# Kernel tuning notes

Hardware: AMD Instinct MI355X
Metric: run time of the kernel (lower is better)

Reference implementation:

```python
import jax, jax.numpy as jnp
import numpy as np

N_NODES = 100000
N_EDGES = 3200000
D_IN = 128
D_OUT = 128


def setup_inputs() -> dict:
    key = jax.random.key(0)
    k1, k2, k3, k4 = jax.random.split(key, 4)
    features = jax.random.normal(k1, (N_NODES, D_IN), dtype=jnp.float32)
    src = jax.random.randint(k2, (N_EDGES,), 0, N_NODES, dtype=jnp.int32)
    dst = jax.random.randint(k3, (N_EDGES,), 0, N_NODES, dtype=jnp.int32)
    # nn.Linear params (Kaiming-uniform-ish init scale)
    bound = 1.0 / np.sqrt(D_IN)
    W = jax.random.uniform(k4, (D_IN, D_OUT), dtype=jnp.float32, minval=-bound, maxval=bound)
    b = jnp.zeros((D_OUT,), dtype=jnp.float32)
    return {"features": features, "W": W, "b": b, "src": src, "dst": dst}


def reference(features, W, b, src, dst):
    # message: gather source node features per edge  [E, D_IN]
    msg = features[src]
    # mean_reduce: segment mean over in-edges per destination node
    summed = jax.ops.segment_sum(msg, dst, num_segments=N_NODES)
    deg = jax.ops.segment_sum(jnp.ones((msg.shape[0],), dtype=features.dtype), dst, num_segments=N_NODES)
    deg = deg[:, None]
    # DGL semantics: nodes with no incoming messages keep their original 'h'
    h = jnp.where(deg > 0, summed / jnp.maximum(deg, 1.0), features)
    # node_update: linear + activation applied to all nodes
    return jax.nn.relu(h @ W + b)
```

## Files before the change

### kernel.cpp

```cpp
#include <hip/hip_runtime.h>

#define N_NODES 100000
#define N_EDGES 3200000
#define D 128

#define BSHIFT 8
#define BSIZE  256
#define NBUCK  391
#define CAP    9216
#define PART_TILE 4096
#define NB_PART ((N_EDGES + PART_TILE - 1) / PART_TILE)
#define CPL 7
#define NSTRIPS (N_NODES / 16)
#define FUSE_GRID 2084

#define OFF_GCUR  0
#define OFF_DBASE 512
#define OFF_OFFS  1024
#define OFF_DEG   101024
#define OFF_CSR   201024
#define FEATB_OFF 13604096ULL
#define WPK_OFF   39204096ULL

typedef __attribute__((ext_vector_type(8))) short short8_t;
typedef __attribute__((ext_vector_type(4))) float f32x4;

__device__ __forceinline__ ushort f2bf(float x) {
    unsigned u = __float_as_uint(x);
    unsigned r = u + 0x7FFFu + ((u >> 16) & 1u);
    return (ushort)(r >> 16);
}
__device__ __forceinline__ float blo(unsigned v) { return __uint_as_float(v << 16); }
__device__ __forceinline__ float bhi(unsigned v) { return __uint_as_float(v & 0xFFFF0000u); }

__global__ __launch_bounds__(256) void gcn_cvt_kernel(
    const float* __restrict__ in, ushort* __restrict__ out, int n8)
{
    int i = blockIdx.x * 256 + threadIdx.x;
    if (i >= n8) return;
    const float4* p = (const float4*)in + (size_t)i * 2;
    float4 a = p[0], b = p[1];
    ushort4 r0 = make_ushort4(f2bf(a.x), f2bf(a.y), f2bf(a.z), f2bf(a.w));
    ushort4 r1 = make_ushort4(f2bf(b.x), f2bf(b.y), f2bf(b.z), f2bf(b.w));
    ushort4* q = (ushort4*)out + (size_t)i * 2;
    q[0] = r0;
    q[1] = r1;
}

__global__ __launch_bounds__(256) void gcn_wpack_kernel(
    const float* __restrict__ W, ushort* __restrict__ wpk)
{
    int tid = blockIdx.x * 256 + threadIdx.x;
    if (tid >= 32 * 64) return;
    int f = tid >> 6, l = tid & 63;
    int n4 = f >> 2, k4 = f & 3;
    int col = n4 * 16 + (l & 15);
    int kb  = k4 * 32 + ((l >> 4) << 3);
    ushort* q = wpk + (size_t)tid * 8;
    #pragma unroll
    for (int t = 0; t < 8; ++t) q[t] = f2bf(W[(kb + t) * D + col]);
}

__global__ void gcn_init_kernel(int* __restrict__ gcur)
{
    int t = blockIdx.x * 256 + threadIdx.x;
    if (t < NBUCK) gcur[t] = t * CAP;
}

__global__ __launch_bounds__(256) void gcn_part_kernel(
    const int* __restrict__ src, const int* __restrict__ dst,
    int* __restrict__ gcur, int* __restrict__ part)
{
    __shared__ int cnt[NBUCK];
    __shared__ int lbase[NBUCK + 1];
    __shared__ int gbase[NBUCK];
    __shared__ int stage[PART_TILE];
    __shared__ ushort sbuck[PART_TILE];

    int t = threadIdx.x;
    int eb = blockIdx.x * PART_TILE;
    int nT = N_EDGES - eb; if (nT > PART_TILE) nT = PART_TILE;

    for (int i = t; i < NBUCK; i += 256) cnt[i] = 0;
    __syncthreads();

    #pragma unroll
    for (int it = 0; it < PART_TILE / 256; ++it) {
        int e = it * 256 + t;
        if (e < nT) atomicAdd(&cnt[dst[eb + e] >> BSHIFT], 1);
    }
    __syncthreads();

    if (t < 64) {
        int v[CPL];
        int s = 0;
        #pragma unroll
        for (int j = 0; j < CPL; ++j) {
            int i = t * CPL + j;
            v[j] = (i < NBUCK) ? cnt[i] : 0;
            s += v[j];
        }
        int inc = s;
        #pragma unroll
        for (int d = 1; d < 64; d <<= 1) {
            int up = __shfl_up(inc, d, 64);
            if (t >= d) inc += up;
        }
        int run = inc - s;
        #pragma unroll
        for (int j = 0; j < CPL; ++j) {
            int i = t * CPL + j;
            if (i < NBUCK) lbase[i] = run;
            run += v[j];
        }
        if (t == 63) lbase[NBUCK] = run;
    }
    __syncthreads();

    for (int i = t; i < NBUCK; i += 256) {
        int c = lbase[i + 1] - lbase[i];
        gbase[i] = c ? atomicAdd(&gcur[i], c) : 0;
        cnt[i] = 0;
    }
    __syncthreads();

    #pragma unroll
    for (int it = 0; it < PART_TILE / 256; ++it) {
        int e = it * 256 + t;
        if (e < nT) {
            int dvv = dst[eb + e];
            int svv = src[eb + e];
            int b  = dvv >> BSHIFT;
            int dl = dvv & (BSIZE - 1);
            int pos = lbase[b] + atomicAdd(&cnt[b], 1);
            stage[pos] = (dl << 17) | svv;
            sbuck[pos] = (ushort)b;
        }
    }
    __syncthreads();

    for (int i = t; i < nT; i += 256) {
        int b = sbuck[i];
        part[gbase[b] + (i - lbase[b])] = stage[i];
    }
}

__global__ __launch_bounds__(64) void gcn_bscan_kernel(
    const int* __restrict__ gcur, int* __restrict__ dbase)
{
    int l = threadIdx.x;
    int v[CPL];
    int s = 0;
    #pragma unroll
    for (int j = 0; j < CPL; ++j) {
        int i = CPL * l + j;
        v[j] = (i < NBUCK) ? (gcur[i] - i * CAP) : 0;
        s += v[j];
    }
    int inc = s;
    #pragma unroll
    for (int d = 1; d < 64; d <<= 1) {
        int up = __shfl_up(inc, d, 64);
        if (l >= d) inc += up;
    }
    int run = inc - s;
    #pragma unroll
    for (int j = 0; j < CPL; ++j) {
        int i = CPL * l + j;
        if (i < NBUCK) dbase[i] = run;
        run += v[j];
    }
}

__global__ __launch_bounds__(256) void gcn_bfill_kernel(
    const int* __restrict__ gcur, const int* __restrict__ dbase,
    const int* __restrict__ part, int* __restrict__ csr,
    int* __restrict__ offs, int* __restrict__ deg)
{
    __shared__ int stage[CAP];
    __shared__ int stage2[CAP];
    __shared__ int ldeg[BSIZE];
    __shared__ int lcur[BSIZE];
    __shared__ int wsum[4];
    int k = blockIdx.x, t = threadIdx.x;
    int pb = k * CAP;
    int nE = gcur[k] - pb;
    if (nE > CAP) nE = CAP;
    int db = dbase[k];

    ldeg[t] = 0;
    __syncthreads();
    for (int i = t; i < nE; i += 256) {
        int pk = part[pb + i];
        stage[i] = pk;
        atomicAdd(&ldeg[pk >> 17], 1);
    }
    __syncthreads();

    int lane = t & 63, wid = t >> 6;
    int v = ldeg[t];
    int inc = v;
    #pragma unroll
    for (int d = 1; d < 64; d <<= 1) {
        int up = __shfl_up(inc, d, 64);
        if (lane >= d) inc += up;
    }
    if (lane == 63) wsum[wid] = inc;
    __syncthreads();
    if (t == 0) {
        int c = 0;
        #pragma unroll
        for (int w = 0; w < 4; ++w) { int x = wsum[w]; wsum[w] = c; c += x; }
    }
    __syncthreads();
    int excl = (inc - v) + wsum[wid];
    lcur[t] = excl;
    int node = (k << BSHIFT) + t;
    if (node < N_NODES) { offs[node] = db + excl; deg[node] = v; }
    __syncthreads();

    for (int i = t; i < nE; i += 256) {
        int pk = stage[i];
        int p = atomicAdd(&lcur[pk >> 17], 1);
        stage2[p] = pk & 0x1FFFF;
    }
    __syncthreads();

    for (int i = t; i < nE; i += 256) csr[db + i] = stage2[i];
}

__global__ __launch_bounds__(256) void gcn_fused_kernel(
    const float* __restrict__ feat,
    const ushort* __restrict__ featb,
    const ushort* __restrict__ wpk,
    const float* __restrict__ bias,
    const int* __restrict__ offs,
    const int* __restrict__ deg,
    const int* __restrict__ csr,
    float* __restrict__ out)
{
    int t = threadIdx.x, lane = t & 63, w = t >> 6;

    short8_t wb[8];
    #pragma unroll
    for (int j = 0; j < 8; ++j)
        wb[j] = *(const short8_t*)(wpk + ((size_t)(w * 8 + j) * 64 + lane) * 8);
    float bj[2];
    bj[0] = bias[(2 * w) * 16 + (lane & 15)];
    bj[1] = bias[(2 * w + 1) * 16 + (lane & 15)];

    __shared__ ushort hlds[16 * 136];

    for (int s = blockIdx.x; s < NSTRIPS; s += FUSE_GRID) {
        int m0 = s * 16;
        __syncthreads();

        #pragma unroll
        for (int i = 0; i < 4; ++i) {
            int r = m0 + w * 4 + i;
            int beg = offs[r], dg = deg[r];
            float s0 = 0.0f, s1 = 0.0f;
            if (dg == 0) {
                float2 f2 = *(const float2*)(feat + (size_t)r * D + lane * 2);
                s0 = f2.x; s1 = f2.y;
            } else {
                int p = beg, e = beg + dg;
                for (; p + 8 <= e; p += 8) {
                    int i0 = csr[p],     i1 = csr[p + 1], i2 = csr[p + 2], i3 = csr[p + 3];
                    int i4 = csr[p + 4], i5 = csr[p + 5], i6 = csr[p + 6], i7 = csr[p + 7];
                    unsigned v0 = *(const unsigned*)(featb + ((size_t)i0 << 7) + lane * 2);
                    unsigned v1 = *(const unsigned*)(featb + ((size_t)i1 << 7) + lane * 2);
                    unsigned v2 = *(const unsigned*)(featb + ((size_t)i2 << 7) + lane * 2);
                    unsigned v3 = *(const unsigned*)(featb + ((size_t)i3 << 7) + lane * 2);
                    unsigned v4 = *(const unsigned*)(featb + ((size_t)i4 << 7) + lane * 2);
                    unsigned v5 = *(const unsigned*)(featb + ((size_t)i5 << 7) + lane * 2);
                    unsigned v6 = *(const unsigned*)(featb + ((size_t)i6 << 7) + lane * 2);
                    unsigned v7 = *(const unsigned*)(featb + ((size_t)i7 << 7) + lane * 2);
                    s0 += blo(v0) + blo(v1) + blo(v2) + blo(v3);
                    s1 += bhi(v0) + bhi(v1) + bhi(v2) + bhi(v3);
                    s0 += blo(v4) + blo(v5) + blo(v6) + blo(v7);
                    s1 += bhi(v4) + bhi(v5) + bhi(v6) + bhi(v7);
                }
                for (; p + 4 <= e; p += 4) {
                    int i0 = csr[p], i1 = csr[p + 1], i2 = csr[p + 2], i3 = csr[p + 3];
                    unsigned v0 = *(const unsigned*)(featb + ((size_t)i0 << 7) + lane * 2);
                    unsigned v1 = *(const unsigned*)(featb + ((size_t)i1 << 7) + lane * 2);
                    unsigned v2 = *(const unsigned*)(featb + ((size_t)i2 << 7) + lane * 2);
                    unsigned v3 = *(const unsigned*)(featb + ((size_t)i3 << 7) + lane * 2);
                    s0 += blo(v0) + blo(v1) + blo(v2) + blo(v3);
                    s1 += bhi(v0) + bhi(v1) + bhi(v2) + bhi(v3);
                }
                for (; p < e; ++p) {
                    unsigned v = *(const unsigned*)(featb + ((size_t)csr[p] << 7) + lane * 2);
                    s0 += blo(v); s1 += bhi(v);
                }
                float inv = 1.0f / (float)dg;
                s0 *= inv; s1 *= inv;
            }
            unsigned pk = ((unsigned)f2bf(s1) << 16) | (unsigned)f2bf(s0);
            *(unsigned*)(&hlds[(w * 4 + i) * 136 + lane * 2]) = pk;
        }
        __syncthreads();

        short8_t a[4];
        #pragma unroll
        for (int k4 = 0; k4 < 4; ++k4)
            a[k4] = *(const short8_t*)(&hlds[(lane & 15) * 136 + k4 * 32 + ((lane >> 4) << 3)]);

        #pragma unroll
        for (int nt = 0; nt < 2; ++nt) {
            f32x4 acc = { bj[nt], bj[nt], bj[nt], bj[nt] };
            #pragma unroll
            for (int k4 = 0; k4 < 4; ++k4)
                acc = __builtin_amdgcn_mfma_f32_16x16x32_bf16(a[k4], wb[nt * 4 + k4], acc, 0, 0, 0);
            int col  = (2 * w + nt) * 16 + (lane & 15);
            int rowb = m0 + ((lane >> 4) << 2);
            #pragma unroll
            for (int rr = 0; rr < 4; ++rr)
                out[(size_t)(rowb + rr) * D + col] = fmaxf(acc[rr], 0.0f);
        }
    }
}

extern "C" void kernel_launch(void* const* d_in, const int* in_sizes, int n_in,
                              void* d_out, int out_size, void* d_ws, size_t ws_size,
                              hipStream_t stream) {
    const float* feat = (const float*)d_in[0];
    const float* W    = (const float*)d_in[1];
    const float* bias = (const float*)d_in[2];
    const int*   src  = (const int*)d_in[3];
    const int*   dst  = (const int*)d_in[4];
    float* out = (float*)d_out;

    int* ib     = (int*)d_ws;
    int* gcur   = ib + OFF_GCUR;
    int* dbase  = ib + OFF_DBASE;
    int* offs   = ib + OFF_OFFS;
    int* deg    = ib + OFF_DEG;
    int* csr    = ib + OFF_CSR;
    ushort* featb = (ushort*)((char*)d_ws + FEATB_OFF);
    ushort* wpk   = (ushort*)((char*)d_ws + WPK_OFF);
    int* part = (int*)d_out;

    {
        int n8 = N_NODES * D / 8;
        gcn_cvt_kernel<<<(n8 + 255) / 256, 256, 0, stream>>>(feat, featb, n8);
    }
    gcn_wpack_kernel<<<8, 256, 0, stream>>>(W, wpk);
    gcn_init_kernel<<<2, 256, 0, stream>>>(gcur);
    gcn_part_kernel<<<NB_PART, 256, 0, stream>>>(src, dst, gcur, part);
    gcn_bscan_kernel<<<1, 64, 0, stream>>>(gcur, dbase);
    gcn_bfill_kernel<<<NBUCK, 256, 0, stream>>>(gcur, dbase, part, csr, offs, deg);
    gcn_fused_kernel<<<FUSE_GRID, 256, 0, stream>>>(feat, featb, wpk, bias, offs, deg, csr, out);
}
```

Measured before the change: 319.8 us.

## Fuse per-bucket CSR build into aggregation kernel using smaller 64-node buckets

Removes the separate bucket-scan and bucket-fill kernels. The fused aggregation kernel now takes one 64-node bucket per block, counting-sorts that bucket's edges in LDS and reads neighbour indices from shared memory instead of a global CSR array. This avoids writing and re-reading the CSR, offsets and degree arrays, and saves two launches. In exchange the partition kernel spreads each tile over 1563 buckets instead of 391, so its global scatter is more fragmented; its tile and thread counts are raised to compensate.

```diff
diff --git a/kernel.cpp b/kernel.cpp
--- a/kernel.cpp
+++ b/kernel.cpp
@@ -4,23 +4,19 @@
 #define N_EDGES 3200000
 #define D 128
 
-#define BSHIFT 8
-#define BSIZE  256
-#define NBUCK  391
-#define CAP    9216
-#define PART_TILE 4096
+#define BSHIFT 6
+#define BNODES 64
+#define NBUCK  1563
+#define CAP    2432
+#define PART_TILE 8192
+#define PART_THREADS 512
 #define NB_PART ((N_EDGES + PART_TILE - 1) / PART_TILE)
-#define CPL 7
-#define NSTRIPS (N_NODES / 16)
-#define FUSE_GRID 2084
+#define CPL 25
 
 #define OFF_GCUR  0
-#define OFF_DBASE 512
-#define OFF_OFFS  1024
-#define OFF_DEG   101024
-#define OFF_CSR   201024
-#define FEATB_OFF 13604096ULL
-#define WPK_OFF   39204096ULL
+#define OFF_PART  2048
+#define FEATB_OFF 15213056ULL
+#define WPK_OFF   40813056ULL
 
 typedef __attribute__((ext_vector_type(8))) short short8_t;
 typedef __attribute__((ext_vector_type(4))) float f32x4;
@@ -67,7 +63,7 @@
     if (t < NBUCK) gcur[t] = t * CAP;
 }
 
-__global__ __launch_bounds__(256) void gcn_part_kernel(
+__global__ __launch_bounds__(PART_THREADS) void gcn_part_kernel(
     const int* __restrict__ src, const int* __restrict__ dst,
     int* __restrict__ gcur, int* __restrict__ part)
 {
@@ -81,12 +77,12 @@
     int eb = blockIdx.x * PART_TILE;
     int nT = N_EDGES - eb; if (nT > PART_TILE) nT = PART_TILE;
 
-    for (int i = t; i < NBUCK; i += 256) cnt[i] = 0;
+    for (int i = t; i < NBUCK; i += PART_THREADS) cnt[i] = 0;
     __syncthreads();
 
     #pragma unroll
-    for (int it = 0; it < PART_TILE / 256; ++it) {
-        int e = it * 256 + t;
+    for (int it = 0; it < PART_TILE / PART_THREADS; ++it) {
+        int e = it * PART_THREADS + t;
         if (e < nT) atomicAdd(&cnt[dst[eb + e] >> BSHIFT], 1);
     }
     __syncthreads();
@@ -117,7 +113,7 @@
     }
     __syncthreads();
 
-    for (int i = t; i < NBUCK; i += 256) {
+    for (int i = t; i < NBUCK; i += PART_THREADS) {
         int c = lbase[i + 1] - lbase[i];
         gbase[i] = c ? atomicAdd(&gcur[i], c) : 0;
         cnt[i] = 0;
@@ -125,13 +121,13 @@
     __syncthreads();
 
     #pragma unroll
-    for (int it = 0; it < PART_TILE / 256; ++it) {
-        int e = it * 256 + t;
+    for (int it = 0; it < PART_TILE / PART_THREADS; ++it) {
+        int e = it * PART_THREADS + t;
         if (e < nT) {
             int dvv = dst[eb + e];
             int svv = src[eb + e];
             int b  = dvv >> BSHIFT;
-            int dl = dvv & (BSIZE - 1);
+            int dl = dvv & (BNODES - 1);
             int pos = lbase[b] + atomicAdd(&cnt[b], 1);
             stage[pos] = (dl << 17) | svv;
             sbuck[pos] = (ushort)b;
@@ -139,94 +135,10 @@
     }
     __syncthreads();
 
-    for (int i = t; i < nT; i += 256) {
+    for (int i = t; i < nT; i += PART_THREADS) {
         int b = sbuck[i];
         part[gbase[b] + (i - lbase[b])] = stage[i];
     }
-}
-
-__global__ __launch_bounds__(64) void gcn_bscan_kernel(
-    const int* __restrict__ gcur, int* __restrict__ dbase)
-{
-    int l = threadIdx.x;
-    int v[CPL];
-    int s = 0;
-    #pragma unroll
-    for (int j = 0; j < CPL; ++j) {
-        int i = CPL * l + j;
-        v[j] = (i < NBUCK) ? (gcur[i] - i * CAP) : 0;
-        s += v[j];
-    }
-    int inc = s;
-    #pragma unroll
-    for (int d = 1; d < 64; d <<= 1) {
-        int up = __shfl_up(inc, d, 64);
-        if (l >= d) inc += up;
-    }
-    int run = inc - s;
-    #pragma unroll
-    for (int j = 0; j < CPL; ++j) {
-        int i = CPL * l + j;
-        if (i < NBUCK) dbase[i] = run;
-        run += v[j];
-    }
-}
-
-__global__ __launch_bounds__(256) void gcn_bfill_kernel(
-    const int* __restrict__ gcur, const int* __restrict__ dbase,
-    const int* __restrict__ part, int* __restrict__ csr,
-    int* __restrict__ offs, int* __restrict__ deg)
-{
-    __shared__ int stage[CAP];
-    __shared__ int stage2[CAP];
-    __shared__ int ldeg[BSIZE];
-    __shared__ int lcur[BSIZE];
-    __shared__ int wsum[4];
-    int k = blockIdx.x, t = threadIdx.x;
-    int pb = k * CAP;
-    int nE = gcur[k] - pb;
-    if (nE > CAP) nE = CAP;
-    int db = dbase[k];
-
-    ldeg[t] = 0;
-    __syncthreads();
-    for (int i = t; i < nE; i += 256) {
-        int pk = part[pb + i];
-        stage[i] = pk;
-        atomicAdd(&ldeg[pk >> 17], 1);
-    }
-    __syncthreads();
-
-    int lane = t & 63, wid = t >> 6;
-    int v = ldeg[t];
-    int inc = v;
-    #pragma unroll
-    for (int d = 1; d < 64; d <<= 1) {
-        int up = __shfl_up(inc, d, 64);
-        if (lane >= d) inc += up;
-    }
-    if (lane == 63) wsum[wid] = inc;
-    __syncthreads();
-    if (t == 0) {
-        int c = 0;
-        #pragma unroll
-        for (int w = 0; w < 4; ++w) { int x = wsum[w]; wsum[w] = c; c += x; }
-    }
-    __syncthreads();
-    int excl = (inc - v) + wsum[wid];
-    lcur[t] = excl;
-    int node = (k << BSHIFT) + t;
-    if (node < N_NODES) { offs[node] = db + excl; deg[node] = v; }
-    __syncthreads();
-
-    for (int i = t; i < nE; i += 256) {
-        int pk = stage[i];
-        int p = atomicAdd(&lcur[pk >> 17], 1);
-        stage2[p] = pk & 0x1FFFF;
-    }
-    __syncthreads();
-
-    for (int i = t; i < nE; i += 256) csr[db + i] = stage2[i];
 }
 
 __global__ __launch_bounds__(256) void gcn_fused_kernel(
@@ -234,12 +146,19 @@
     const ushort* __restrict__ featb,
     const ushort* __restrict__ wpk,
     const float* __restrict__ bias,
-    const int* __restrict__ offs,
-    const int* __restrict__ deg,
-    const int* __restrict__ csr,
+    const int* __restrict__ gcur,
+    const int* __restrict__ part,
     float* __restrict__ out)
 {
+    __shared__ int stage[CAP];
+    __shared__ int stage2[CAP];
+    __shared__ int ldeg[BNODES];
+    __shared__ int loff[BNODES];
+    __shared__ int lcur[BNODES];
+    __shared__ ushort hlds[16 * 136];
+
     int t = threadIdx.x, lane = t & 63, w = t >> 6;
+    int k = blockIdx.x;
 
     short8_t wb[8];
     #pragma unroll
@@ -249,53 +168,87 @@
     bj[0] = bias[(2 * w) * 16 + (lane & 15)];
     bj[1] = bias[(2 * w + 1) * 16 + (lane & 15)];
 
-    __shared__ ushort hlds[16 * 136];
-
-    for (int s = blockIdx.x; s < NSTRIPS; s += FUSE_GRID) {
-        int m0 = s * 16;
+    int pb = k * CAP;
+    int nE = gcur[k] - pb;
+    if (nE > CAP) nE = CAP;
+
+    if (t < BNODES) ldeg[t] = 0;
+    __syncthreads();
+
+    for (int i = t; i < nE; i += 256) {
+        int pk = part[pb + i];
+        stage[i] = pk;
+        atomicAdd(&ldeg[pk >> 17], 1);
+    }
+    __syncthreads();
+
+    if (t < 64) {
+        int v = ldeg[t];
+        int inc = v;
+        #pragma unroll
+        for (int d = 1; d < 64; d <<= 1) {
+            int up = __shfl_up(inc, d, 64);
+            if (t >= d) inc += up;
+        }
+        loff[t] = inc - v;
+        lcur[t] = inc - v;
+    }
+    __syncthreads();
+
+    for (int i = t; i < nE; i += 256) {
+        int pk = stage[i];
+        int p = atomicAdd(&lcur[pk >> 17], 1);
+        stage2[p] = pk & 0x1FFFF;
+    }
+
+    #pragma unroll 1
+    for (int si = 0; si < 4; ++si) {
         __syncthreads();
 
         #pragma unroll
         for (int i = 0; i < 4; ++i) {
-            int r = m0 + w * 4 + i;
-            int beg = offs[r], dg = deg[r];
+            int nl = si * 16 + w * 4 + i;
+            int r  = k * BNODES + nl;
             float s0 = 0.0f, s1 = 0.0f;
-            if (dg == 0) {
-                float2 f2 = *(const float2*)(feat + (size_t)r * D + lane * 2);
-                s0 = f2.x; s1 = f2.y;
-            } else {
-                int p = beg, e = beg + dg;
-                for (; p + 8 <= e; p += 8) {
-                    int i0 = csr[p],     i1 = csr[p + 1], i2 = csr[p + 2], i3 = csr[p + 3];
-                    int i4 = csr[p + 4], i5 = csr[p + 5], i6 = csr[p + 6], i7 = csr[p + 7];
-                    unsigned v0 = *(const unsigned*)(featb + ((size_t)i0 << 7) + lane * 2);
-                    unsigned v1 = *(const unsigned*)(featb + ((size_t)i1 << 7) + lane * 2);
-                    unsigned v2 = *(const unsigned*)(featb + ((size_t)i2 << 7) + lane * 2);
-                    unsigned v3 = *(const unsigned*)(featb + ((size_t)i3 << 7) + lane * 2);
-                    unsigned v4 = *(const unsigned*)(featb + ((size_t)i4 << 7) + lane * 2);
-                    unsigned v5 = *(const unsigned*)(featb + ((size_t)i5 << 7) + lane * 2);
-                    unsigned v6 = *(const unsigned*)(featb + ((size_t)i6 << 7) + lane * 2);
-                    unsigned v7 = *(const unsigned*)(featb + ((size_t)i7 << 7) + lane * 2);
-                    s0 += blo(v0) + blo(v1) + blo(v2) + blo(v3);
-                    s1 += bhi(v0) + bhi(v1) + bhi(v2) + bhi(v3);
-                    s0 += blo(v4) + blo(v5) + blo(v6) + blo(v7);
-                    s1 += bhi(v4) + bhi(v5) + bhi(v6) + bhi(v7);
+            if (r < N_NODES) {
+                int dg = ldeg[nl], beg = loff[nl];
+                if (dg == 0) {
+                    float2 f2 = *(const float2*)(feat + (size_t)r * D + lane * 2);
+                    s0 = f2.x; s1 = f2.y;
+                } else {
+                    int p = beg, e = beg + dg;
+                    for (; p + 8 <= e; p += 8) {
+                        int i0 = stage2[p],     i1 = stage2[p + 1], i2 = stage2[p + 2], i3 = stage2[p + 3];
+                        int i4 = stage2[p + 4], i5 = stage2[p + 5], i6 = stage2[p + 6], i7 = stage2[p + 7];
+                        unsigned v0 = *(const unsigned*)(featb + ((size_t)i0 << 7) + lane * 2);
+                        unsigned v1 = *(const unsigned*)(featb + ((size_t)i1 << 7) + lane * 2);
+                        unsigned v2 = *(const unsigned*)(featb + ((size_t)i2 << 7) + lane * 2);
+                        unsigned v3 = *(const unsigned*)(featb + ((size_t)i3 << 7) + lane * 2);
+                        unsigned v4 = *(const unsigned*)(featb + ((size_t)i4 << 7) + lane * 2);
+                        unsigned v5 = *(const unsigned*)(featb + ((size_t)i5 << 7) + lane * 2);
+                        unsigned v6 = *(const unsigned*)(featb + ((size_t)i6 << 7) + lane * 2);
+                        unsigned v7 = *(const unsigned*)(featb + ((size_t)i7 << 7) + lane * 2);
+                        s0 += blo(v0) + blo(v1) + blo(v2) + blo(v3);
+                        s1 += bhi(v0) + bhi(v1) + bhi(v2) + bhi(v3);
+                        s0 += blo(v4) + blo(v5) + blo(v6) + blo(v7);
+                        s1 += bhi(v4) + bhi(v5) + bhi(v6) + bhi(v7);
+                    }
+                    for (; p + 4 <= e; p += 4) {
+                        int i0 = stage2[p], i1 = stage2[p + 1], i2 = stage2[p + 2], i3 = stage2[p + 3];
+                        unsigned v0 = *(const unsigned*)(featb + ((size_t)i0 << 7) + lane * 2);
+                        unsigned v1 = *(const unsigned*)(featb + ((size_t)i1 << 7) + lane * 2);
+                        unsigned v2 = *(const unsigned*)(featb + ((size_t)i2 << 7) + lane * 2);
+                        unsigned v3 = *(const unsigned*)(featb + ((size_t)i3 << 7) + lane * 2);
+                        s0 += blo(v0) + blo(v1) + blo(v2) + blo(v3);
+                        s1 += bhi(v0) + bhi(v1) + bhi(v2) + bhi(v3);
+                    }
+                    for (; p < e; ++p) {
+                        unsigned v = *(const unsigned*)(featb + ((size_t)stage2[p] << 7) + lane * 2);
+                        s0 += blo(v); s1 += bhi(v);
+                    }
+                    float inv = 1.0f / (float)dg;
+                    s0 *= inv; s1 *= inv;
                 }
-                for (; p + 4 <= e; p += 4) {
-                    int i0 = csr[p], i1 = csr[p + 1], i2 = csr[p + 2], i3 = csr[p + 3];
-                    unsigned v0 = *(const unsigned*)(featb + ((size_t)i0 << 7) + lane * 2);
-                    unsigned v1 = *(const unsigned*)(featb + ((size_t)i1 << 7) + lane * 2);
-                    unsigned v2 = *(const unsigned*)(featb + ((size_t)i2 << 7) + lane * 2);
-                    unsigned v3 = *(const unsigned*)(featb + ((size_t)i3 << 7) + lane * 2);
-                    s0 += blo(v0) + blo(v1) + blo(v2) + blo(v3);
-                    s1 += bhi(v0) + bhi(v1) + bhi(v2) + bhi(v3);
-                }
-                for (; p < e; ++p) {
-                    unsigned v = *(const unsigned*)(featb + ((size_t)csr[p] << 7) + lane * 2);
-                    s0 += blo(v); s1 += bhi(v);
-                }
-                float inv = 1.0f / (float)dg;
-                s0 *= inv; s1 *= inv;
             }
             unsigned pk = ((unsigned)f2bf(s1) << 16) | (unsigned)f2bf(s0);
             *(unsigned*)(&hlds[(w * 4 + i) * 136 + lane * 2]) = pk;
@@ -307,17 +260,18 @@
         for (int k4 = 0; k4 < 4; ++k4)
             a[k4] = *(const short8_t*)(&hlds[(lane & 15) * 136 + k4 * 32 + ((lane >> 4) << 3)]);
 
+        int rowb = k * BNODES + si * 16 + ((lane >> 4) << 2);
         #pragma unroll
         for (int nt = 0; nt < 2; ++nt) {
             f32x4 acc = { bj[nt], bj[nt], bj[nt], bj[nt] };
             #pragma unroll
             for (int k4 = 0; k4 < 4; ++k4)
                 acc = __builtin_amdgcn_mfma_f32_16x16x32_bf16(a[k4], wb[nt * 4 + k4], acc, 0, 0, 0);
-            int col  = (2 * w + nt) * 16 + (lane & 15);
-            int rowb = m0 + ((lane >> 4) << 2);
+            int col = (2 * w + nt) * 16 + (lane & 15);
             #pragma unroll
             for (int rr = 0; rr < 4; ++rr)
-                out[(size_t)(rowb + rr) * D + col] = fmaxf(acc[rr], 0.0f);
+                if (rowb + rr < N_NODES)
+                    out[(size_t)(rowb + rr) * D + col] = fmaxf(acc[rr], 0.0f);
         }
     }
 }
@@ -332,24 +286,18 @@
     const int*   dst  = (const int*)d_in[4];
     float* out = (float*)d_out;
 
-    int* ib     = (int*)d_ws;
-    int* gcur   = ib + OFF_GCUR;
-    int* dbase  = ib + OFF_DBASE;
-    int* offs   = ib + OFF_OFFS;
-    int* deg    = ib + OFF_DEG;
-    int* csr    = ib + OFF_CSR;
+    int* ib   = (int*)d_ws;
+    int* gcur = ib + OFF_GCUR;
+    int* part = ib + OFF_PART;
     ushort* featb = (ushort*)((char*)d_ws + FEATB_OFF);
     ushort* wpk   = (ushort*)((char*)d_ws + WPK_OFF);
-    int* part = (int*)d_out;
 
     {
         int n8 = N_NODES * D / 8;
         gcn_cvt_kernel<<<(n8 + 255) / 256, 256, 0, stream>>>(feat, featb, n8);
     }
     gcn_wpack_kernel<<<8, 256, 0, stream>>>(W, wpk);
-    gcn_init_kernel<<<2, 256, 0, stream>>>(gcur);
-    gcn_part_kernel<<<NB_PART, 256, 0, stream>>>(src, dst, gcur, part);
-    gcn_bscan_kernel<<<1, 64, 0, stream>>>(gcur, dbase);
-    gcn_bfill_kernel<<<NBUCK, 256, 0, stream>>>(gcur, dbase, part, csr, offs, deg);
-    gcn_fused_kernel<<<FUSE_GRID, 256, 0, stream>>>(feat, featb, wpk, bias, offs, deg, csr, out);
-}
+    gcn_init_kernel<<<(NBUCK + 255) / 256, 256, 0, stream>>>(gcur);
+    gcn_part_kernel<<<NB_PART, PART_THREADS, 0, stream>>>(src, dst, gcur, part);
+    gcn_fused_kernel<<<NBUCK, 256, 0, stream>>>(feat, featb, wpk, bias, gcur, part, out);
+}
```

Measured after the change: 289.9 us. -9.4%, faster.
